# Performance work log

Hardware: AMD Instinct MI355X
Metric: run time of the kernel (lower is better)

The kernel has to match this reference:

```python
import math
import jax, jax.numpy as jnp
import numpy as np


def setup_inputs() -> dict:
    key = jax.random.key(0)
    k1, k2 = jax.random.split(key)
    b, t, h, d = 2, 2048, 16, 64
    q = jax.random.normal(k1, (b, t, h, d), dtype=jnp.float32)
    kv = jax.random.normal(k2, (b, t, 2, h, d), dtype=jnp.float32)
    return {"q": q, "kv": kv}


def reference(q, kv):
    # Padded cross-attention branch, causal=False, dropout=0 (identity).
    d = q.shape[-1]
    softmax_scale = 1.0 / math.sqrt(d)
    k = kv[:, :, 0]  # [b, s, h, d]
    v = kv[:, :, 1]  # [b, s, h, d]
    # scores: [b, h, t, s] -- full score matrix, matching torch einsum
    scores = jnp.einsum('bthd,bshd->bhts', q, k * softmax_scale)
    attention = jax.nn.softmax(scores, axis=-1)
    out = jnp.einsum('bhts,bshd->bthd', attention, v)
    return out
```

## Files before the change

### kernel.cpp

```cpp
#include <hip/hip_runtime.h>
#include <hip/hip_bf16.h>

typedef __attribute__((ext_vector_type(8)))  short v8s;
typedef __attribute__((ext_vector_type(4)))  float v4f;
typedef __attribute__((ext_vector_type(16))) float v16f;
typedef unsigned long long u64;
typedef unsigned short u16;

#define BB 2
#define TT 2048
#define HH 16
#define DD 64


__device__ __forceinline__ unsigned short f2bf(float f) {
    unsigned int u = __builtin_bit_cast(unsigned int, f);
    u = u + 0x7FFFu + ((u >> 16) & 1u);
    return (unsigned short)(u >> 16);
}

__device__ __forceinline__ unsigned cvt2(float a, float b) {
    return ((unsigned)f2bf(b) << 16) | (unsigned)f2bf(a);
}

__device__ __forceinline__ v8s cvt8s(const float4& lo, const float4& hi, float s) {
    union { v8s v; unsigned u[4]; } r;
    r.u[0] = cvt2(lo.x * s, lo.y * s);
    r.u[1] = cvt2(lo.z * s, lo.w * s);
    r.u[2] = cvt2(hi.x * s, hi.y * s);
    r.u[3] = cvt2(hi.z * s, hi.w * s);
    return r.v;
}

__device__ __forceinline__ unsigned cvtpk(float lo, float hi) {
    unsigned r;
    asm("v_cvt_pk_bf16_f32 %0, %1, %2" : "=v"(r) : "v"(lo), "v"(hi));
    return r;
}

__device__ __forceinline__ v8s pack8(u64 lo, u64 hi) {
    union { v8s v; u64 q[2]; } u;
    u.q[0] = lo; u.q[1] = hi;
    return u.v;
}

typedef __attribute__((address_space(1))) const unsigned int gas_u32;
typedef __attribute__((address_space(3))) unsigned int las_u32;
__device__ __forceinline__ void gl_lds16(const void* g, void* l) {
    __builtin_amdgcn_global_load_lds((gas_u32*)g, (las_u32*)l, 16, 0, 0);
}


__global__ __launch_bounds__(256)
void prep_kv(const float* __restrict__ kvg, u16* __restrict__ wsK, u16* __restrict__ wsV) {
    __shared__ u16 vlds[64][72];
    const int wg   = blockIdx.x;
    const int tile = wg & 31;
    const int h    = (wg >> 5) & 15;
    const int b    = wg >> 9;
    const int t    = threadIdx.x;
    const int s0   = tile * 64;

    u16* kout = wsK + (((size_t)(b * 16 + h) * 32 + tile) * 4096);
    u16* vout = wsV + (((size_t)(b * 16 + h) * 32 + tile) * 4096);

    #pragma unroll
    for (int i = 0; i < 2; ++i) {
        int id  = t + 256 * i;
        int row = id >> 3;
        int bi  = id & 7;
        int c   = bi >> 1, hh = bi & 1;
        const float* kp = kvg + ((((size_t)(b * TT + s0 + row) * 2 + 0) * HH + h) * DD + 16 * c + 4 * hh);
        float4 ka = *(const float4*)kp;
        float4 kb = *(const float4*)(kp + 8);
        *(v8s*)((char*)kout + row * 128 + ((bi ^ (row & 7)) << 4)) = cvt8s(ka, kb, 1.0f);
    }
    #pragma unroll
    for (int i = 0; i < 2; ++i) {
        int id  = t + 256 * i;
        int row = id >> 3;
        int d8  = id & 7;
        const float* vp = kvg + ((((size_t)(b * TT + s0 + row) * 2 + 1) * HH + h) * DD + 8 * d8);
        float4 va = *(const float4*)vp;
        float4 vb = *(const float4*)(vp + 4);
        *(v8s*)&vlds[row][8 * d8] = cvt8s(va, vb, 1.0f);
    }
    __syncthreads();
    #pragma unroll
    for (int i = 0; i < 2; ++i) {
        int id = t + 256 * i;
        int dd = id >> 3;
        int bi = id & 7;
        int cc = bi >> 1, hh = bi & 1;
        union { v8s v; u16 w[8]; } r;
        #pragma unroll
        for (int j = 0; j < 4; ++j) {
            r.w[j]     = vlds[16 * cc + 4 * hh + j][dd];
            r.w[4 + j] = vlds[16 * cc + 8 + 4 * hh + j][dd];
        }
        *(v8s*)((char*)vout + dd * 128 + ((bi ^ (dd & 7)) << 4)) = r.v;
    }
}


__global__ __launch_bounds__(256, 2)
void attn_v5(const float* __restrict__ qg, const u16* __restrict__ wsK,
             const u16* __restrict__ wsV, float* __restrict__ outg) {
    __shared__ __align__(16) u16 KT[2][4096];
    __shared__ __align__(16) u16 VT[2][4096];

    const int bid  = blockIdx.x;
    const int wgid = (bid & 7) * 64 + (bid >> 3);
    const int qt   = wgid & 15;
    const int hH   = (wgid >> 4) & 15;
    const int b    = wgid >> 8;
    const int tid  = threadIdx.x;
    const int lane = tid & 63;
    const int wid  = tid >> 6;
    const int al   = lane & 31;
    const int hh   = lane >> 5;

    const u16* kbase = wsK + (size_t)(b * 16 + hH) * 131072;
    const u16* vbase = wsV + (size_t)(b * 16 + hH) * 131072;

    const int q0 = qt * 128 + wid * 32;
    const int qr = q0 + al;

    const float qscale = 0.125f * 1.4426950408889634f;
    v8s qf[4];
    {
        const float* qb = qg + ((size_t)((b * TT + qr) * HH + hH)) * DD;
        #pragma unroll
        for (int c = 0; c < 4; ++c) {
            float4 lo = *(const float4*)(qb + 16 * c + 4 * hh);
            float4 hi = *(const float4*)(qb + 16 * c + 4 * hh + 8);
            qf[c] = cvt8s(lo, hi, qscale);
        }
    }

#define STAGE(buf, tt)                                                                                    \
    do {                                                                                                  \
        gl_lds16(kbase + (size_t)(tt) * 4096 + tid * 8,        (char*)&KT[buf][0] + wid * 1024);          \
        gl_lds16(kbase + (size_t)(tt) * 4096 + 2048 + tid * 8, (char*)&KT[buf][0] + 4096 + wid * 1024);   \
        gl_lds16(vbase + (size_t)(tt) * 4096 + tid * 8,        (char*)&VT[buf][0] + wid * 1024);          \
        gl_lds16(vbase + (size_t)(tt) * 4096 + 2048 + tid * 8, (char*)&VT[buf][0] + 4096 + wid * 1024);   \
    } while (0)

    STAGE(0, 0);

    v16f oa[2];
    #pragma unroll
    for (int dt = 0; dt < 2; ++dt)
        #pragma unroll
        for (int r = 0; r < 16; ++r) oa[dt][r] = 0.0f;
    float m = -INFINITY, lsum = 0.0f;

    for (int t = 0; t < 32; ++t) {
        const int cur = t & 1;
        if (t < 31) {
            STAGE(cur ^ 1, t + 1);
            asm volatile("s_waitcnt vmcnt(4)" ::: "memory");
        } else {
            asm volatile("s_waitcnt vmcnt(0)" ::: "memory");
        }
        __builtin_amdgcn_s_barrier();

        const char* kb = (const char*)&KT[cur][0];
        const char* vb = (const char*)&VT[cur][0];

        v16f st[2];
        #pragma unroll
        for (int kt = 0; kt < 2; ++kt)
            #pragma unroll
            for (int r = 0; r < 16; ++r) st[kt][r] = 0.0f;
        __builtin_amdgcn_s_setprio(1);
        #pragma unroll
        for (int c = 0; c < 4; ++c) {
            #pragma unroll
            for (int kt = 0; kt < 2; ++kt) {
                int row = 32 * kt + al;
                v8s kf = *(const v8s*)(kb + row * 128 + (((2 * c + hh) ^ (row & 7)) << 4));
                st[kt] = __builtin_amdgcn_mfma_f32_32x32x16_bf16(kf, qf[c], st[kt], 0, 0, 0);
            }
        }
        __builtin_amdgcn_s_setprio(0);

        float mc = st[0][0];
        #pragma unroll
        for (int kt = 0; kt < 2; ++kt)
            #pragma unroll
            for (int r = 0; r < 16; ++r) mc = fmaxf(mc, st[kt][r]);
        mc = fmaxf(mc, __shfl_xor(mc, 32));
        if (!__all(mc - m <= 8.0f)) {
            float mnew  = fmaxf(m, mc);
            float alpha = __builtin_amdgcn_exp2f(m - mnew);
            lsum *= alpha;
            m = mnew;
            #pragma unroll
            for (int dt = 0; dt < 2; ++dt)
                #pragma unroll
                for (int r = 0; r < 16; ++r) oa[dt][r] *= alpha;
        }
        float ps = 0.0f;
        #pragma unroll
        for (int kt = 0; kt < 2; ++kt)
            #pragma unroll
            for (int r = 0; r < 16; ++r) {
                float e = __builtin_amdgcn_exp2f(st[kt][r] - m);
                st[kt][r] = e;
                ps += e;
            }
        ps += __shfl_xor(ps, 32);
        lsum += ps;

        v8s pf[4];
        #pragma unroll
        for (int cc = 0; cc < 4; ++cc) {
            const int kt = cc >> 1, u8 = 8 * (cc & 1);
            union { v8s v; unsigned u[4]; } r;
            #pragma unroll
            for (int w = 0; w < 4; ++w)
                r.u[w] = cvtpk(st[kt][u8 + 2 * w], st[kt][u8 + 2 * w + 1]);
            pf[cc] = r.v;
        }

        __builtin_amdgcn_s_setprio(1);
        #pragma unroll
        for (int cc = 0; cc < 4; ++cc) {
            #pragma unroll
            for (int dt = 0; dt < 2; ++dt) {
                int row = 32 * dt + al;
                v8s vf = *(const v8s*)(vb + row * 128 + (((2 * cc + hh) ^ (row & 7)) << 4));
                oa[dt] = __builtin_amdgcn_mfma_f32_32x32x16_bf16(vf, pf[cc], oa[dt], 0, 0, 0);
            }
        }
        __builtin_amdgcn_s_setprio(0);

        __builtin_amdgcn_s_barrier();
    }

    float rl = 1.0f / lsum;
    const size_t obase = ((size_t)((b * TT + qr) * HH + hH)) * DD;
    #pragma unroll
    for (int dt = 0; dt < 2; ++dt)
        #pragma unroll
        for (int r = 0; r < 16; ++r) {
            int d = 32 * dt + (r & 3) + 8 * (r >> 2) + 4 * hh;
            outg[obase + d] = oa[dt][r] * rl;
        }
}


__global__ __launch_bounds__(256)
void attn_fwd_v1(const float* __restrict__ qg, const float* __restrict__ kvg,
                 float* __restrict__ outg) {
    __shared__ __align__(16) u16 Klds[32][68];
    __shared__ __align__(16) u16 Vt[DD][36];

    const int wg    = blockIdx.x;
    const int qtile = wg & 31;
    const int h     = (wg >> 5) & 15;
    const int b     = wg >> 9;
    const int tid   = threadIdx.x;
    const int lane  = tid & 63;
    const int wid   = tid >> 6;
    const int lr    = lane & 15;
    const int lg    = lane >> 4;
    const int q0    = qtile * 64 + wid * 16;

    const float qscale = 0.125f * 1.4426950408889634f;
    v8s qf[2];
    {
        const float* qb = qg + ((size_t)((b * TT + q0 + lr) * HH + h)) * DD;
        #pragma unroll
        for (int c = 0; c < 2; ++c) {
            float4 lo = *(const float4*)(qb + 32 * c + 4 * lg);
            float4 hi = *(const float4*)(qb + 32 * c + 4 * lg + 16);
            qf[c] = cvt8s(lo, hi, qscale);
        }
    }

    v4f oa[4];
    #pragma unroll
    for (int dc = 0; dc < 4; ++dc)
        #pragma unroll
        for (int r = 0; r < 4; ++r) oa[dc][r] = 0.0f;
    float m = -INFINITY, lsum = 0.0f;

    for (int kv0 = 0; kv0 < TT; kv0 += 32) {
        __syncthreads();
        #pragma unroll
        for (int i = 0; i < 2; ++i) {
            int id  = tid + 256 * i;
            int row = id >> 4;
            int cg  = (id & 15) * 4;
            const float* gp = kvg + ((size_t)(((b * TT + kv0 + row) * 2 + 0) * HH + h)) * DD + cg;
            float4 f = *(const float4*)gp;
            ushort4 w;
            w.x = f2bf(f.x); w.y = f2bf(f.y); w.z = f2bf(f.z); w.w = f2bf(f.w);
            *(ushort4*)&Klds[row][cg] = w;
        }
        {
            int s0 = tid >> 4;
            int dg = (tid & 15) * 4;
            const float* gp0 = kvg + ((size_t)(((b * TT + kv0 + 2 * s0) * 2 + 1) * HH + h)) * DD + dg;
            const float* gp1 = gp0 + 2 * HH * DD;
            float4 fa = *(const float4*)gp0;
            float4 fb = *(const float4*)gp1;
            float av[4] = {fa.x, fa.y, fa.z, fa.w};
            float bv[4] = {fb.x, fb.y, fb.z, fb.w};
            #pragma unroll
            for (int i = 0; i < 4; ++i) {
                ushort2 w;
                w.x = f2bf(av[i]);
                w.y = f2bf(bv[i]);
                *(ushort2*)&Vt[dg + i][2 * s0] = w;
            }
        }
        __syncthreads();

        v4f st0, st1;
        #pragma unroll
        for (int r = 0; r < 4; ++r) { st0[r] = 0.0f; st1[r] = 0.0f; }
        #pragma unroll
        for (int c = 0; c < 2; ++c) {
            {
                u64 lo = *(const u64*)&Klds[lr][32 * c + 4 * lg];
                u64 hi = *(const u64*)&Klds[lr][32 * c + 4 * lg + 16];
                st0 = __builtin_amdgcn_mfma_f32_16x16x32_bf16(pack8(lo, hi), qf[c], st0, 0, 0, 0);
            }
            {
                u64 lo = *(const u64*)&Klds[16 + lr][32 * c + 4 * lg];
                u64 hi = *(const u64*)&Klds[16 + lr][32 * c + 4 * lg + 16];
                st1 = __builtin_amdgcn_mfma_f32_16x16x32_bf16(pack8(lo, hi), qf[c], st1, 0, 0, 0);
            }
        }

        float sc[8] = {st0[0], st0[1], st0[2], st0[3], st1[0], st1[1], st1[2], st1[3]};
        float mc = sc[0];
        #pragma unroll
        for (int i = 1; i < 8; ++i) mc = fmaxf(mc, sc[i]);
        mc = fmaxf(mc, __shfl_xor(mc, 16));
        mc = fmaxf(mc, __shfl_xor(mc, 32));
        float mnew  = fmaxf(m, mc);
        float alpha = __builtin_amdgcn_exp2f(m - mnew);
        float p[8], ps = 0.0f;
        #pragma unroll
        for (int i = 0; i < 8; ++i) { p[i] = __builtin_amdgcn_exp2f(sc[i] - mnew); ps += p[i]; }
        ps += __shfl_xor(ps, 16);
        ps += __shfl_xor(ps, 32);
        lsum = lsum * alpha + ps;
        m = mnew;

        float ar0 = __shfl(alpha, 4 * lg + 0);
        float ar1 = __shfl(alpha, 4 * lg + 1);
        float ar2 = __shfl(alpha, 4 * lg + 2);
        float ar3 = __shfl(alpha, 4 * lg + 3);
        #pragma unroll
        for (int dc = 0; dc < 4; ++dc) {
            oa[dc][0] *= ar0; oa[dc][1] *= ar1; oa[dc][2] *= ar2; oa[dc][3] *= ar3;
        }

        v8s pf;
        #pragma unroll
        for (int i = 0; i < 8; ++i) pf[i] = (short)f2bf(p[i]);

        #pragma unroll
        for (int dc = 0; dc < 4; ++dc) {
            u64 lo = *(const u64*)&Vt[16 * dc + lr][4 * lg];
            u64 hi = *(const u64*)&Vt[16 * dc + lr][4 * lg + 16];
            oa[dc] = __builtin_amdgcn_mfma_f32_16x16x32_bf16(pf, pack8(lo, hi), oa[dc], 0, 0, 0);
        }
    }

    float rl  = 1.0f / lsum;
    float rr0 = __shfl(rl, 4 * lg + 0);
    float rr1 = __shfl(rl, 4 * lg + 1);
    float rr2 = __shfl(rl, 4 * lg + 2);
    float rr3 = __shfl(rl, 4 * lg + 3);
    #pragma unroll
    for (int dc = 0; dc < 4; ++dc) {
        size_t base = ((size_t)((b * TT + q0) * HH + h)) * DD + 16 * dc + lr;
        outg[base + (size_t)(4 * lg + 0) * HH * DD] = oa[dc][0] * rr0;
        outg[base + (size_t)(4 * lg + 1) * HH * DD] = oa[dc][1] * rr1;
        outg[base + (size_t)(4 * lg + 2) * HH * DD] = oa[dc][2] * rr2;
        outg[base + (size_t)(4 * lg + 3) * HH * DD] = oa[dc][3] * rr3;
    }
}

extern "C" void kernel_launch(void* const* d_in, const int* in_sizes, int n_in,
                              void* d_out, int out_size, void* d_ws, size_t ws_size,
                              hipStream_t stream) {
    const float* q  = (const float*)d_in[0];
    const float* kv = (const float*)d_in[1];
    float* out      = (float*)d_out;
    if (ws_size >= (size_t)16777216) {
        u16* wsK = (u16*)d_ws;
        u16* wsV = wsK + 4194304;
        hipLaunchKernelGGL(prep_kv, dim3(BB * HH * 32), dim3(256), 0, stream, kv, wsK, wsV);
        hipLaunchKernelGGL(attn_v5, dim3(512), dim3(256), 0, stream, q, wsK, wsV, out);
    } else {
        hipLaunchKernelGGL(attn_fwd_v1, dim3(1024), dim3(256), 0, stream, q, kv, out);
    }
}
```

Baseline: 65.03 us.

## Split KV sequence across wave pairs and merge partial softmax results in LDS

The attention kernel now gives each workgroup 64 query rows and splits the KV sequence in half between two pairs of waves. Each pair runs online softmax over its half with 32-key tiles, and the two partial results are merged through LDS at the end. The grid grows from 512 to 1024 blocks, and launch bounds now ask for 4 blocks per CU to raise occupancy. The prep kernel writes K and V in a new 32-row swizzled tile layout to match. The cost is a final LDS reduction step and less reuse of each KV tile, since it is now loaded for 64 query rows instead of 128, which doubles global KV traffic.

```diff
diff --git a/kernel.cpp b/kernel.cpp
--- a/kernel.cpp
+++ b/kernel.cpp
@@ -55,32 +55,34 @@
 void prep_kv(const float* __restrict__ kvg, u16* __restrict__ wsK, u16* __restrict__ wsV) {
     __shared__ u16 vlds[64][72];
     const int wg   = blockIdx.x;
-    const int tile = wg & 31;
+    const int t64  = wg & 31;
     const int h    = (wg >> 5) & 15;
     const int b    = wg >> 9;
     const int t    = threadIdx.x;
-    const int s0   = tile * 64;
-
-    u16* kout = wsK + (((size_t)(b * 16 + h) * 32 + tile) * 4096);
-    u16* vout = wsV + (((size_t)(b * 16 + h) * 32 + tile) * 4096);
+    const int s0g  = t64 * 64;
+
+    char* kout = (char*)(wsK + ((size_t)(b * 16 + h) * 131072)) + t64 * 8192;
+    char* vout = (char*)(wsV + ((size_t)(b * 16 + h) * 131072)) + t64 * 8192;
 
     #pragma unroll
     for (int i = 0; i < 2; ++i) {
-        int id  = t + 256 * i;
-        int row = id >> 3;
-        int bi  = id & 7;
-        int c   = bi >> 1, hh = bi & 1;
-        const float* kp = kvg + ((((size_t)(b * TT + s0 + row) * 2 + 0) * HH + h) * DD + 16 * c + 4 * hh);
+        int id   = t + 256 * i;
+        int row  = id >> 3;
+        int bi   = id & 7;
+        int c    = bi >> 1, hh = bi & 1;
+        const float* kp = kvg + ((((size_t)(b * TT + s0g + row) * 2 + 0) * HH + h) * DD + 16 * c + 4 * hh);
         float4 ka = *(const float4*)kp;
         float4 kb = *(const float4*)(kp + 8);
-        *(v8s*)((char*)kout + row * 128 + ((bi ^ (row & 7)) << 4)) = cvt8s(ka, kb, 1.0f);
+        int tt2 = row >> 5, s = row & 31;
+        int blk = (((c << 2) | (((s >> 4) & 1) << 1) | hh) ^ (s & 7));
+        *(v8s*)(kout + tt2 * 4096 + (s & 15) * 256 + (blk << 4)) = cvt8s(ka, kb, 1.0f);
     }
     #pragma unroll
     for (int i = 0; i < 2; ++i) {
         int id  = t + 256 * i;
         int row = id >> 3;
         int d8  = id & 7;
-        const float* vp = kvg + ((((size_t)(b * TT + s0 + row) * 2 + 1) * HH + h) * DD + 8 * d8);
+        const float* vp = kvg + ((((size_t)(b * TT + s0g + row) * 2 + 1) * HH + h) * DD + 8 * d8);
         float4 va = *(const float4*)vp;
         float4 vb = *(const float4*)(vp + 4);
         *(v8s*)&vlds[row][8 * d8] = cvt8s(va, vb, 1.0f);
@@ -88,62 +90,84 @@
     __syncthreads();
     #pragma unroll
     for (int i = 0; i < 2; ++i) {
-        int id = t + 256 * i;
-        int dd = id >> 3;
-        int bi = id & 7;
-        int cc = bi >> 1, hh = bi & 1;
+        int id  = t + 256 * i;
+        int tt2 = id >> 8;
+        int dd  = (id >> 2) & 63;
+        int cc  = (id >> 1) & 1;
+        int hh  = id & 1;
+        int s0l = 32 * tt2;
         union { v8s v; u16 w[8]; } r;
         #pragma unroll
         for (int j = 0; j < 4; ++j) {
-            r.w[j]     = vlds[16 * cc + 4 * hh + j][dd];
-            r.w[4 + j] = vlds[16 * cc + 8 + 4 * hh + j][dd];
-        }
-        *(v8s*)((char*)vout + dd * 128 + ((bi ^ (dd & 7)) << 4)) = r.v;
-    }
-}
-
-
-__global__ __launch_bounds__(256, 2)
-void attn_v5(const float* __restrict__ qg, const u16* __restrict__ wsK,
+            r.w[j]     = vlds[s0l + 16 * cc + 4 * hh + j][dd];
+            r.w[4 + j] = vlds[s0l + 16 * cc + 8 + 4 * hh + j][dd];
+        }
+        int blk = (((cc << 2) | (((dd >> 4) & 1) << 1) | hh) ^ (dd & 7));
+        *(v8s*)(vout + tt2 * 4096 + (dd >> 5) * 2048 + (dd & 15) * 128 + (blk << 4)) = r.v;
+    }
+}
+
+
+__global__ __launch_bounds__(256, 4)
+void attn_v6(const float* __restrict__ qg, const u16* __restrict__ wsK,
              const u16* __restrict__ wsV, float* __restrict__ outg) {
-    __shared__ __align__(16) u16 KT[2][4096];
-    __shared__ __align__(16) u16 VT[2][4096];
+    __shared__ __align__(16) char smem[32768];
 
     const int bid  = blockIdx.x;
-    const int wgid = (bid & 7) * 64 + (bid >> 3);
-    const int qt   = wgid & 15;
-    const int hH   = (wgid >> 4) & 15;
-    const int b    = wgid >> 8;
+    const int wgid = (bid & 7) * 128 + (bid >> 3);
+    const int qb   = wgid & 31;
+    const int hH   = (wgid >> 5) & 15;
+    const int b    = wgid >> 9;
     const int tid  = threadIdx.x;
     const int lane = tid & 63;
-    const int wid  = tid >> 6;
+    const int w    = tid >> 6;
+    const int qh   = w & 1;
+    const int g    = w >> 1;
     const int al   = lane & 31;
+    const int a4   = al >> 4;
     const int hh   = lane >> 5;
-
-    const u16* kbase = wsK + (size_t)(b * 16 + hH) * 131072;
-    const u16* vbase = wsV + (size_t)(b * 16 + hH) * 131072;
-
-    const int q0 = qt * 128 + wid * 32;
+    const int gtid = tid & 127;
+
+    const char* kbase = (const char*)(wsK + (size_t)(b * 16 + hH) * 131072) + g * 131072;
+    const char* vbase = (const char*)(wsV + (size_t)(b * 16 + hH) * 131072) + g * 131072;
+
+    char* Kg = smem + g * 16384;
+    char* Vg = smem + g * 16384 + 8192;
+
+    const int q0 = qb * 64 + qh * 32;
     const int qr = q0 + al;
 
     const float qscale = 0.125f * 1.4426950408889634f;
     v8s qf[4];
     {
-        const float* qb = qg + ((size_t)((b * TT + qr) * HH + hH)) * DD;
+        const float* qp = qg + ((size_t)((b * TT + qr) * HH + hH)) * DD;
         #pragma unroll
         for (int c = 0; c < 4; ++c) {
-            float4 lo = *(const float4*)(qb + 16 * c + 4 * hh);
-            float4 hi = *(const float4*)(qb + 16 * c + 4 * hh + 8);
+            float4 lo = *(const float4*)(qp + 16 * c + 4 * hh);
+            float4 hi = *(const float4*)(qp + 16 * c + 4 * hh + 8);
             qf[c] = cvt8s(lo, hi, qscale);
         }
     }
 
-#define STAGE(buf, tt)                                                                                    \
-    do {                                                                                                  \
-        gl_lds16(kbase + (size_t)(tt) * 4096 + tid * 8,        (char*)&KT[buf][0] + wid * 1024);          \
-        gl_lds16(kbase + (size_t)(tt) * 4096 + 2048 + tid * 8, (char*)&KT[buf][0] + 4096 + wid * 1024);   \
-        gl_lds16(vbase + (size_t)(tt) * 4096 + tid * 8,        (char*)&VT[buf][0] + wid * 1024);          \
-        gl_lds16(vbase + (size_t)(tt) * 4096 + 2048 + tid * 8, (char*)&VT[buf][0] + 4096 + wid * 1024);   \
+    const int kswz = (a4 << 1) | hh;
+    int koff[4], voff[2][2];
+    #pragma unroll
+    for (int c = 0; c < 4; ++c)
+        koff[c] = (al & 15) * 256 + ((((c << 2) | kswz) ^ (al & 7)) << 4);
+    #pragma unroll
+    for (int dt = 0; dt < 2; ++dt)
+        #pragma unroll
+        for (int cc = 0; cc < 2; ++cc)
+            voff[dt][cc] = dt * 2048 + (al & 15) * 128 + ((((cc << 2) | kswz) ^ (al & 7)) << 4);
+
+#define STAGE(buf, ii)                                                         \
+    do {                                                                       \
+        const char* ks = kbase + (size_t)(ii) * 4096;                          \
+        const char* vs = vbase + (size_t)(ii) * 4096;                          \
+        gl_lds16(ks + gtid * 16,        Kg + (buf) * 4096 + qh * 1024);        \
+        gl_lds16(ks + 2048 + gtid * 16, Kg + (buf) * 4096 + 2048 + qh * 1024); \
+        gl_lds16(vs + gtid * 16,        Vg + (buf) * 4096 + qh * 1024);        \
+        gl_lds16(vs + 2048 + gtid * 16, Vg + (buf) * 4096 + 2048 + qh * 1024); \
     } while (0)
 
     STAGE(0, 0);
@@ -155,41 +179,33 @@
         for (int r = 0; r < 16; ++r) oa[dt][r] = 0.0f;
     float m = -INFINITY, lsum = 0.0f;
 
-    for (int t = 0; t < 32; ++t) {
-        const int cur = t & 1;
-        if (t < 31) {
-            STAGE(cur ^ 1, t + 1);
+    for (int i = 0; i < 32; ++i) {
+        const int cur = i & 1;
+        if (i < 31) {
+            STAGE(cur ^ 1, i + 1);
             asm volatile("s_waitcnt vmcnt(4)" ::: "memory");
         } else {
             asm volatile("s_waitcnt vmcnt(0)" ::: "memory");
         }
         __builtin_amdgcn_s_barrier();
 
-        const char* kb = (const char*)&KT[cur][0];
-        const char* vb = (const char*)&VT[cur][0];
-
-        v16f st[2];
-        #pragma unroll
-        for (int kt = 0; kt < 2; ++kt)
-            #pragma unroll
-            for (int r = 0; r < 16; ++r) st[kt][r] = 0.0f;
+        const char* kb = Kg + cur * 4096;
+        const char* vb = Vg + cur * 4096;
+
+        v16f st;
+        #pragma unroll
+        for (int r = 0; r < 16; ++r) st[r] = 0.0f;
         __builtin_amdgcn_s_setprio(1);
         #pragma unroll
         for (int c = 0; c < 4; ++c) {
-            #pragma unroll
-            for (int kt = 0; kt < 2; ++kt) {
-                int row = 32 * kt + al;
-                v8s kf = *(const v8s*)(kb + row * 128 + (((2 * c + hh) ^ (row & 7)) << 4));
-                st[kt] = __builtin_amdgcn_mfma_f32_32x32x16_bf16(kf, qf[c], st[kt], 0, 0, 0);
-            }
+            v8s kf = *(const v8s*)(kb + koff[c]);
+            st = __builtin_amdgcn_mfma_f32_32x32x16_bf16(kf, qf[c], st, 0, 0, 0);
         }
         __builtin_amdgcn_s_setprio(0);
 
-        float mc = st[0][0];
-        #pragma unroll
-        for (int kt = 0; kt < 2; ++kt)
-            #pragma unroll
-            for (int r = 0; r < 16; ++r) mc = fmaxf(mc, st[kt][r]);
+        float mc = st[0];
+        #pragma unroll
+        for (int r = 1; r < 16; ++r) mc = fmaxf(mc, st[r]);
         mc = fmaxf(mc, __shfl_xor(mc, 32));
         if (!__all(mc - m <= 8.0f)) {
             float mnew  = fmaxf(m, mc);
@@ -203,34 +219,30 @@
         }
         float ps = 0.0f;
         #pragma unroll
-        for (int kt = 0; kt < 2; ++kt)
-            #pragma unroll
-            for (int r = 0; r < 16; ++r) {
-                float e = __builtin_amdgcn_exp2f(st[kt][r] - m);
-                st[kt][r] = e;
-                ps += e;
-            }
+        for (int r = 0; r < 16; ++r) {
+            float e = __builtin_amdgcn_exp2f(st[r] - m);
+            st[r] = e;
+            ps += e;
+        }
         ps += __shfl_xor(ps, 32);
         lsum += ps;
 
-        v8s pf[4];
-        #pragma unroll
-        for (int cc = 0; cc < 4; ++cc) {
-            const int kt = cc >> 1, u8 = 8 * (cc & 1);
+        v8s pf[2];
+        #pragma unroll
+        for (int cc = 0; cc < 2; ++cc) {
             union { v8s v; unsigned u[4]; } r;
             #pragma unroll
-            for (int w = 0; w < 4; ++w)
-                r.u[w] = cvtpk(st[kt][u8 + 2 * w], st[kt][u8 + 2 * w + 1]);
+            for (int ww = 0; ww < 4; ++ww)
+                r.u[ww] = cvtpk(st[8 * cc + 2 * ww], st[8 * cc + 2 * ww + 1]);
             pf[cc] = r.v;
         }
 
         __builtin_amdgcn_s_setprio(1);
         #pragma unroll
-        for (int cc = 0; cc < 4; ++cc) {
+        for (int cc = 0; cc < 2; ++cc) {
             #pragma unroll
             for (int dt = 0; dt < 2; ++dt) {
-                int row = 32 * dt + al;
-                v8s vf = *(const v8s*)(vb + row * 128 + (((2 * cc + hh) ^ (row & 7)) << 4));
+                v8s vf = *(const v8s*)(vb + voff[dt][cc]);
                 oa[dt] = __builtin_amdgcn_mfma_f32_32x32x16_bf16(vf, pf[cc], oa[dt], 0, 0, 0);
             }
         }
@@ -239,15 +251,34 @@
         __builtin_amdgcn_s_barrier();
     }
 
-    float rl = 1.0f / lsum;
-    const size_t obase = ((size_t)((b * TT + qr) * HH + hH)) * DD;
-    #pragma unroll
-    for (int dt = 0; dt < 2; ++dt)
-        #pragma unroll
-        for (int r = 0; r < 16; ++r) {
-            int d = 32 * dt + (r & 3) + 8 * (r >> 2) + 4 * hh;
-            outg[obase + d] = oa[dt][r] * rl;
-        }
+    __syncthreads();
+    float* mg = (float*)smem;
+    if (g == 1) {
+        float* p = mg + (qh * 64 + lane) * 34;
+        #pragma unroll
+        for (int dt = 0; dt < 2; ++dt)
+            #pragma unroll
+            for (int r = 0; r < 16; ++r) p[dt * 16 + r] = oa[dt][r];
+        p[32] = m;
+        p[33] = lsum;
+    }
+    __syncthreads();
+    if (g == 0) {
+        const float* p = mg + (qh * 64 + lane) * 34;
+        float m1 = p[32], l1 = p[33];
+        float ms = fmaxf(m, m1);
+        float a0 = __builtin_amdgcn_exp2f(m - ms);
+        float a1 = __builtin_amdgcn_exp2f(m1 - ms);
+        float li = 1.0f / (lsum * a0 + l1 * a1);
+        const size_t obase = ((size_t)((b * TT + qr) * HH + hH)) * DD;
+        #pragma unroll
+        for (int dt = 0; dt < 2; ++dt)
+            #pragma unroll
+            for (int r = 0; r < 16; ++r) {
+                int d = 32 * dt + (r & 3) + 8 * (r >> 2) + 4 * hh;
+                outg[obase + d] = (oa[dt][r] * a0 + p[dt * 16 + r] * a1) * li;
+            }
+    }
 }
 
 
@@ -398,7 +429,7 @@
         u16* wsK = (u16*)d_ws;
         u16* wsV = wsK + 4194304;
         hipLaunchKernelGGL(prep_kv, dim3(BB * HH * 32), dim3(256), 0, stream, kv, wsK, wsV);
-        hipLaunchKernelGGL(attn_v5, dim3(512), dim3(256), 0, stream, q, wsK, wsV, out);
+        hipLaunchKernelGGL(attn_v6, dim3(1024), dim3(256), 0, stream, q, wsK, wsV, out);
     } else {
         hipLaunchKernelGGL(attn_fwd_v1, dim3(1024), dim3(256), 0, stream, q, kv, out);
     }
```

Measured after the change: 68.25 us. 4.9% more time.
